# Performance work log

Measured on AMD Instinct MI355X. Metric: run time of the kernel, lower is better.

The kernel has to match this reference:

```python
import jax, jax.numpy as jnp
import numpy as np

N, E, F_IN, ED, H, C, G, ACT = 50000, 800000, 32, 5, 2, 32, 128, 8
HC = H * C


def _glorot(key, shape):
    fan_in, fan_out = shape[0], shape[-1]
    lim = (6.0 / (fan_in + fan_out)) ** 0.5
    return jax.random.uniform(key, shape, jnp.float32, -lim, lim)


def setup_inputs() -> dict:
    key = jax.random.key(0)
    ks = jax.random.split(key, 32)
    inp = {
        "x": jax.random.normal(ks[0], (N, F_IN), jnp.float32),
        "edge_index": jax.random.randint(ks[1], (2, E), 0, N, jnp.int64),
        "edge_attr": jax.random.normal(ks[2], (E, ED), jnp.float32),
        "batch": jnp.sort(jax.random.randint(ks[3], (N,), 0, G, jnp.int64)),
    }
    ki = 4
    for l, din in zip((1, 2, 3), (F_IN, HC, HC)):
        inp[f"W{l}"] = _glorot(ks[ki], (din, HC)); ki += 1
        inp[f"We{l}"] = _glorot(ks[ki], (ED, HC)); ki += 1
        inp[f"as{l}"] = _glorot(ks[ki], (H, C)); ki += 1
        inp[f"ad{l}"] = _glorot(ks[ki], (H, C)); ki += 1
        inp[f"ae{l}"] = _glorot(ks[ki], (H, C)); ki += 1
        inp[f"b{l}"] = jnp.zeros((HC,), jnp.float32)
    inp["Wl"] = _glorot(ks[ki], (HC, ACT)); ki += 1
    inp["bl"] = jnp.zeros((ACT,), jnp.float32)
    return inp


def _add_self_loops(edge_index, edge_attr):
    # PyG add_self_loops with fill_value='mean': self-loop edge_attr at node i
    # is the mean of edge_attr of edges whose dst is i (0 if none).
    dst = edge_index[1]
    deg = jax.ops.segment_sum(jnp.ones((E,), jnp.float32), dst, num_segments=N)
    loop_attr = jax.ops.segment_sum(edge_attr, dst, num_segments=N) / jnp.clip(deg, 1.0)[:, None]
    loops = jnp.arange(N, dtype=edge_index.dtype)
    ei = jnp.concatenate([edge_index, jnp.stack([loops, loops])], axis=1)
    ea = jnp.concatenate([edge_attr, loop_attr], axis=0)
    return ei, ea


def _gat_layer(x, src, dst, ea, W, We, a_s, a_d, a_e, b):
    xs = (x @ W).reshape(N, H, C)                      # node features per head
    e = (ea @ We).reshape(-1, H, C)                    # edge features per head
    a_src = jnp.einsum('nhc,hc->nh', xs, a_s)
    a_dst = jnp.einsum('nhc,hc->nh', xs, a_d)
    a_edge = jnp.einsum('ehc,hc->eh', e, a_e)
    logits = jax.nn.leaky_relu(a_src[src] + a_dst[dst] + a_edge, 0.2)  # [E',H]
    m = jax.ops.segment_max(logits, dst, num_segments=N)
    m = jnp.where(jnp.isfinite(m), m, 0.0)
    ex = jnp.exp(logits - m[dst])
    den = jax.ops.segment_sum(ex, dst, num_segments=N)
    alpha = ex / (den[dst] + 1e-16)
    msg = xs[src] * alpha[..., None]                   # [E',H,C]
    out = jax.ops.segment_sum(msg, dst, num_segments=N).reshape(N, HC)
    return out + b


def reference(x, edge_index, edge_attr, batch,
              W1, We1, as1, ad1, ae1, b1,
              W2, We2, as2, ad2, ae2, b2,
              W3, We3, as3, ad3, ae3, b3,
              Wl, bl):
    ei, ea = _add_self_loops(edge_index, edge_attr)
    src, dst = ei[0], ei[1]
    h = jax.nn.relu(_gat_layer(x, src, dst, ea, W1, We1, as1, ad1, ae1, b1))
    h = jax.nn.relu(_gat_layer(h, src, dst, ea, W2, We2, as2, ad2, ae2, b2))
    h = _gat_layer(h, src, dst, ea, W3, We3, as3, ad3, ae3, b3)
    # global mean pool over graphs
    cnt = jax.ops.segment_sum(jnp.ones((N,), jnp.float32), batch, num_segments=G)
    pooled = jax.ops.segment_sum(h, batch, num_segments=G) / jnp.clip(cnt, 1.0)[:, None]
    return jnp.tanh(pooled @ Wl + bl)
```

## Files before the change

kernel.cpp:

```cpp
#include <hip/hip_runtime.h>
#include <math.h>

#define N_NODES 50000
#define N_EDGES 800000
#define E_DIM   5
#define N_G     128
#define N_ACT   8
#define SBLK    512
#define SNB     ((N_NODES + SBLK - 1) / SBLK)


__global__ __launch_bounds__(256) void setup_kernel(
    const int* __restrict__ ei, const int* __restrict__ batch,
    const float* __restrict__ We1, const float* __restrict__ ae1,
    const float* __restrict__ We2, const float* __restrict__ ae2,
    const float* __restrict__ We3, const float* __restrict__ ae3,
    float* __restrict__ weff, int* __restrict__ gstart, int* __restrict__ hist) {
    int bid = blockIdx.x, tid = threadIdx.x;
    if (bid == 0) {
        if (tid <= N_G) {
            int g = tid, lo = 0, hi = N_NODES;
            while (lo < hi) { int mid = (lo + hi) >> 1; if (batch[mid] < g) lo = mid + 1; else hi = mid; }
            gstart[g] = lo;
        }
        int t = tid - 160;
        if (t >= 0 && t < 30) {
            int l = t / 10, r = t % 10, d = r >> 1, h = r & 1;
            const float* We = (l == 0) ? We1 : (l == 1) ? We2 : We3;
            const float* ae = (l == 0) ? ae1 : (l == 1) ? ae2 : ae3;
            float s = 0.f;
            for (int c = 0; c < 32; ++c) s += We[d * 64 + h * 32 + c] * ae[h * 32 + c];
            weff[l * 10 + d * 2 + h] = s;
        }
        return;
    }
    int k = (bid - 1) * 256 + tid;
    if (k < N_EDGES) atomicAdd(&hist[ei[N_EDGES + k]], 1);
}

__device__ __forceinline__ int wave_incl_scan(int v, int lane) {
    #pragma unroll
    for (int off = 1; off < 64; off <<= 1) {
        int n = __shfl_up(v, off);
        if (lane >= off) v += n;
    }
    return v;
}

__global__ __launch_bounds__(SBLK) void scan_bsum_kernel(const int* __restrict__ hist,
                                                         int* __restrict__ bsum) {
    int i = blockIdx.x * SBLK + threadIdx.x;
    int v = (i < N_NODES) ? hist[i] : 0;
    __shared__ int sm[SBLK / 64];
    int lane = threadIdx.x & 63, w = threadIdx.x >> 6;
    #pragma unroll
    for (int o = 32; o; o >>= 1) v += __shfl_xor(v, o);
    if (lane == 0) sm[w] = v;
    __syncthreads();
    if (threadIdx.x == 0) {
        int s = 0;
        #pragma unroll
        for (int k = 0; k < SBLK / 64; ++k) s += sm[k];
        bsum[blockIdx.x] = s;
    }
}

__global__ __launch_bounds__(SBLK) void scan_rowptr_kernel(const int* __restrict__ hist,
                                                           const int* __restrict__ bsum,
                                                           int* __restrict__ rowptr) {
    __shared__ int s_boffs;
    __shared__ int wtot[SBLK / 64];
    int bid = blockIdx.x;
    if (threadIdx.x < 64) {
        int v = 0;
        for (int i = threadIdx.x; i < bid; i += 64) v += bsum[i];
        #pragma unroll
        for (int o = 32; o; o >>= 1) v += __shfl_xor(v, o);
        if (threadIdx.x == 0) s_boffs = v;
    }
    int i = bid * SBLK + threadIdx.x;
    int v = (i < N_NODES) ? hist[i] : 0;
    int lane = threadIdx.x & 63, w = threadIdx.x >> 6;
    int inc = wave_incl_scan(v, lane);
    if (lane == 63) wtot[w] = inc;
    __syncthreads();
    int woff = 0;
    for (int k = 0; k < w; ++k) woff += wtot[k];
    int excl = s_boffs + woff + inc - v;
    if (i < N_NODES) rowptr[i] = excl;
    if (i == N_NODES - 1) rowptr[N_NODES] = excl + v;
}

__global__ void scatter_kernel(const int* __restrict__ ei, const float* __restrict__ ea,
                               const float* __restrict__ weff,
                               const int* __restrict__ rowptr, int* __restrict__ cur,
                               float* __restrict__ rec) {
    int k = blockIdx.x * blockDim.x + threadIdx.x;
    if (k >= N_EDGES) return;
    int s = ei[k], d = ei[N_EDGES + k];
    const float* ep = ea + (size_t)k * E_DIM;
    float e[5];
    #pragma unroll
    for (int j = 0; j < 5; ++j) e[j] = ep[j];
    float r[6] = {0.f, 0.f, 0.f, 0.f, 0.f, 0.f};
    #pragma unroll
    for (int j = 0; j < 5; ++j) {
        r[0] += e[j] * weff[j * 2];      r[1] += e[j] * weff[j * 2 + 1];
        r[2] += e[j] * weff[10 + j * 2]; r[3] += e[j] * weff[10 + j * 2 + 1];
        r[4] += e[j] * weff[20 + j * 2]; r[5] += e[j] * weff[20 + j * 2 + 1];
    }
    int pos = rowptr[d] + atomicAdd(&cur[d], 1);
    float4* rp = (float4*)(rec + (size_t)pos * 8);
    rp[0] = make_float4(r[0], r[1], r[2], r[3]);
    rp[1] = make_float4(r[4], r[5], __int_as_float(s), 0.f);
}


template <int DIN>
__global__ __launch_bounds__(256) void feat_kernel(
    const float* __restrict__ in, const float* __restrict__ W,
    const float* __restrict__ a_s, const float* __restrict__ a_d,
    float* __restrict__ xs, float* __restrict__ a_srcv, float* __restrict__ a_dstv) {
    __shared__ float Wl[DIN * 64];
    __shared__ float asl[64], adl[64];
    int tid = threadIdx.x;
    {
        const float4* Wg = (const float4*)W;
        float4* Wl4 = (float4*)Wl;
        #pragma unroll
        for (int i = tid; i < DIN * 16; i += 256) Wl4[i] = Wg[i];
        if (tid < 64) { asl[tid] = a_s[tid]; adl[tid] = a_d[tid]; }
    }
    __syncthreads();
    int n = blockIdx.x * 64 + (tid >> 2);
    int strip = tid & 3;
    if (n >= N_NODES) return;
    float4 xr[DIN / 4];
    const float4* row4 = (const float4*)(in + (size_t)n * DIN);
    #pragma unroll
    for (int k4 = 0; k4 < DIN / 4; ++k4) xr[k4] = row4[k4];
    float4 acc[4];
    #pragma unroll
    for (int j = 0; j < 4; ++j) acc[j] = make_float4(0.f, 0.f, 0.f, 0.f);
    const float4* W4 = (const float4*)Wl;
    #pragma unroll
    for (int k4 = 0; k4 < DIN / 4; ++k4) {
        float xk[4] = {xr[k4].x, xr[k4].y, xr[k4].z, xr[k4].w};
        #pragma unroll
        for (int kk = 0; kk < 4; ++kk) {
            int k = k4 * 4 + kk;
            #pragma unroll
            for (int j = 0; j < 4; ++j) {
                float4 w = W4[k * 16 + strip * 4 + j];
                acc[j].x += xk[kk] * w.x; acc[j].y += xk[kk] * w.y;
                acc[j].z += xk[kk] * w.z; acc[j].w += xk[kk] * w.w;
            }
        }
    }
    float ps = 0.f, pd = 0.f;
    #pragma unroll
    for (int j = 0; j < 4; ++j) {
        int c = strip * 16 + j * 4;
        ps += acc[j].x * asl[c] + acc[j].y * asl[c + 1] + acc[j].z * asl[c + 2] + acc[j].w * asl[c + 3];
        pd += acc[j].x * adl[c] + acc[j].y * adl[c + 1] + acc[j].z * adl[c + 2] + acc[j].w * adl[c + 3];
    }
    ps += __shfl_xor(ps, 1);
    pd += __shfl_xor(pd, 1);
    if ((strip & 1) == 0) {
        int h = strip >> 1;
        a_srcv[n * 2 + h] = ps;
        a_dstv[n * 2 + h] = pd;
    }
    float4* o = (float4*)(xs + (size_t)n * 64 + strip * 16);
    #pragma unroll
    for (int j = 0; j < 4; ++j) o[j] = acc[j];
}

template <int L>
__global__ __launch_bounds__(256) void node_agg_kernel(
    const int* __restrict__ rowptr, const float* __restrict__ rec,
    const float* __restrict__ a_srcv, const float* __restrict__ a_dstv,
    const float* __restrict__ xs, const float* __restrict__ b,
    float* __restrict__ out, int relu) {
    int nid = (blockIdx.x * 256 + threadIdx.x) >> 4;
    if (nid >= N_NODES) return;
    int lane = threadIdx.x & 63;
    int fl = lane & 15, h = fl >> 3;
    int gbase = lane & 48;
    int beg = rowptr[nid], end = rowptr[nid + 1];
    float2 ad2 = ((const float2*)a_dstv)[nid];

    float m0 = -INFINITY, m1 = -INFINITY, d0 = 0.f, d1 = 0.f;
    float aes0 = 0.f, aes1 = 0.f;
    for (int j = beg + fl; j < end; j += 16) {
        const float4* rp = (const float4*)(rec + (size_t)j * 8);
        float4 r0 = rp[0];
        float4 r1 = rp[1];
        int s = __float_as_int(r1.z);
        float aex = (L == 0) ? r0.x : (L == 1) ? r0.z : r1.x;
        float aey = (L == 0) ? r0.y : (L == 1) ? r0.w : r1.y;
        aes0 += aex; aes1 += aey;
        float2 as2 = ((const float2*)a_srcv)[s];
        float l0 = as2.x + ad2.x + aex;
        float l1 = as2.y + ad2.y + aey;
        l0 = (l0 > 0.f) ? l0 : 0.2f * l0;
        l1 = (l1 > 0.f) ? l1 : 0.2f * l1;
        float n0 = fmaxf(m0, l0);
        d0 = d0 * __expf(m0 - n0) + __expf(l0 - n0); m0 = n0;
        float n1 = fmaxf(m1, l1);
        d1 = d1 * __expf(m1 - n1) + __expf(l1 - n1); m1 = n1;
    }
    #pragma unroll
    for (int o = 8; o; o >>= 1) {
        float mo0 = __shfl_xor(m0, o), do0 = __shfl_xor(d0, o);
        float mo1 = __shfl_xor(m1, o), do1 = __shfl_xor(d1, o);
        float n0 = fmaxf(m0, mo0);
        float ea0 = (m0 == n0) ? 1.f : __expf(m0 - n0);
        float eb0 = (mo0 == n0) ? 1.f : __expf(mo0 - n0);
        d0 = d0 * ea0 + do0 * eb0; m0 = n0;
        float n1 = fmaxf(m1, mo1);
        float ea1 = (m1 == n1) ? 1.f : __expf(m1 - n1);
        float eb1 = (mo1 == n1) ? 1.f : __expf(mo1 - n1);
        d1 = d1 * ea1 + do1 * eb1; m1 = n1;
        aes0 += __shfl_xor(aes0, o);
        aes1 += __shfl_xor(aes1, o);
    }
    int ne = end - beg;
    float invne = 1.f / fmaxf((float)ne, 1.f);
    float2 as2n = ((const float2*)a_srcv)[nid];
    float ls0 = as2n.x + ad2.x + aes0 * invne;
    float ls1 = as2n.y + ad2.y + aes1 * invne;
    ls0 = (ls0 > 0.f) ? ls0 : 0.2f * ls0;
    ls1 = (ls1 > 0.f) ? ls1 : 0.2f * ls1;
    float M0 = fmaxf(m0, ls0), M1 = fmaxf(m1, ls1);
    float sc0 = (m0 == M0) ? 1.f : __expf(m0 - M0);
    float sc1 = (m1 == M1) ? 1.f : __expf(m1 - M1);
    float exS0 = __expf(ls0 - M0), exS1 = __expf(ls1 - M1);
    float den0 = d0 * sc0 + exS0;
    float den1 = d1 * sc1 + exS1;

    float4 acc = make_float4(0.f, 0.f, 0.f, 0.f);
    for (int cb = beg; cb < end; cb += 16) {
        int j = cb + fl;
        float ex0 = 0.f, ex1 = 0.f;
        int s = 0;
        if (j < end) {
            const float4* rp = (const float4*)(rec + (size_t)j * 8);
            float4 r0 = rp[0];
            float4 r1 = rp[1];
            s = __float_as_int(r1.z);
            float aex = (L == 0) ? r0.x : (L == 1) ? r0.z : r1.x;
            float aey = (L == 0) ? r0.y : (L == 1) ? r0.w : r1.y;
            float2 as2 = ((const float2*)a_srcv)[s];
            float l0 = as2.x + ad2.x + aex;
            float l1 = as2.y + ad2.y + aey;
            l0 = (l0 > 0.f) ? l0 : 0.2f * l0;
            l1 = (l1 > 0.f) ? l1 : 0.2f * l1;
            ex0 = __expf(l0 - M0);
            ex1 = __expf(l1 - M1);
        }
        int cnt = min(end - cb, 16);
        for (int t4 = 0; t4 < cnt; t4 += 4) {
            int tA = gbase + t4;
            float eA0 = __shfl(ex0, tA),     eA1 = __shfl(ex1, tA);     int sA = __shfl(s, tA);
            float eB0 = __shfl(ex0, tA + 1), eB1 = __shfl(ex1, tA + 1); int sB = __shfl(s, tA + 1);
            float eC0 = __shfl(ex0, tA + 2), eC1 = __shfl(ex1, tA + 2); int sC = __shfl(s, tA + 2);
            float eD0 = __shfl(ex0, tA + 3), eD1 = __shfl(ex1, tA + 3); int sD = __shfl(s, tA + 3);
            float eA = h ? eA1 : eA0, eB = h ? eB1 : eB0;
            float eC = h ? eC1 : eC0, eD = h ? eD1 : eD0;
            float4 xa = *(const float4*)(xs + (size_t)sA * 64 + fl * 4);
            float4 xb = *(const float4*)(xs + (size_t)sB * 64 + fl * 4);
            float4 xc = *(const float4*)(xs + (size_t)sC * 64 + fl * 4);
            float4 xd = *(const float4*)(xs + (size_t)sD * 64 + fl * 4);
            acc.x += eA * xa.x + eB * xb.x + eC * xc.x + eD * xd.x;
            acc.y += eA * xa.y + eB * xb.y + eC * xc.y + eD * xd.y;
            acc.z += eA * xa.z + eB * xb.z + eC * xc.z + eD * xd.z;
            acc.w += eA * xa.w + eB * xb.w + eC * xc.w + eD * xd.w;
        }
    }
    float exSh = h ? exS1 : exS0;
    float den  = (h ? den1 : den0) + 1e-16f;
    float4 xv = *(const float4*)(xs + (size_t)nid * 64 + fl * 4);
    float inv = 1.f / den;
    float4 b4 = ((const float4*)b)[fl];
    float4 v;
    v.x = (acc.x + exSh * xv.x) * inv + b4.x;
    v.y = (acc.y + exSh * xv.y) * inv + b4.y;
    v.z = (acc.z + exSh * xv.z) * inv + b4.z;
    v.w = (acc.w + exSh * xv.w) * inv + b4.w;
    if (relu) {
        v.x = fmaxf(v.x, 0.f); v.y = fmaxf(v.y, 0.f);
        v.z = fmaxf(v.z, 0.f); v.w = fmaxf(v.w, 0.f);
    }
    ((float4*)(out + (size_t)nid * 64))[fl] = v;
}


__global__ __launch_bounds__(256) void pool_head_kernel(
    const float* __restrict__ hfeat, const int* __restrict__ gstart,
    const float* __restrict__ Wl, const float* __restrict__ bl,
    float* __restrict__ out) {
    __shared__ float sm[4][64];
    __shared__ float pooledL[64];
    int g = blockIdx.x;
    int w = threadIdx.x >> 6, lane = threadIdx.x & 63;
    int beg = gstart[g], end = gstart[g + 1];
    float acc = 0.f;
    for (int n = beg + w; n < end; n += 4)
        acc += hfeat[(size_t)n * 64 + lane];
    sm[w][lane] = acc;
    __syncthreads();
    if (w == 0) {
        float v = sm[0][lane] + sm[1][lane] + sm[2][lane] + sm[3][lane];
        pooledL[lane] = v / fmaxf((float)(end - beg), 1.f);
    }
    __syncthreads();
    if (threadIdx.x < N_ACT) {
        int a = threadIdx.x;
        float s = bl[a];
        #pragma unroll
        for (int j = 0; j < 64; ++j) s += pooledL[j] * Wl[j * 8 + a];
        out[g * N_ACT + a] = tanhf(s);
    }
}

extern "C" void kernel_launch(void* const* d_in, const int* in_sizes, int n_in,
                              void* d_out, int out_size, void* d_ws, size_t ws_size,
                              hipStream_t stream) {
    const float* x    = (const float*)d_in[0];
    const int*   ei   = (const int*)d_in[1];
    const float* ea   = (const float*)d_in[2];
    const int*   batch= (const int*)d_in[3];
    const float* W[3]   = {(const float*)d_in[4],  (const float*)d_in[10], (const float*)d_in[16]};
    const float* We[3]  = {(const float*)d_in[5],  (const float*)d_in[11], (const float*)d_in[17]};
    const float* as_[3] = {(const float*)d_in[6],  (const float*)d_in[12], (const float*)d_in[18]};
    const float* ad_[3] = {(const float*)d_in[7],  (const float*)d_in[13], (const float*)d_in[19]};
    const float* ae_[3] = {(const float*)d_in[8],  (const float*)d_in[14], (const float*)d_in[20]};
    const float* b_[3]  = {(const float*)d_in[9],  (const float*)d_in[15], (const float*)d_in[21]};
    const float* Wlin = (const float*)d_in[22];
    const float* bl   = (const float*)d_in[23];
    float* out = (float*)d_out;

    float* ws = (float*)d_ws;
    size_t off = 0;
    float* A      = ws + off; off += (size_t)N_NODES * 64;
    float* B      = ws + off; off += (size_t)N_NODES * 64;
    float* rec    = ws + off; off += (size_t)N_EDGES * 8;
    float* a_srcv = ws + off; off += N_NODES * 2;
    float* a_dstv = ws + off; off += N_NODES * 2;
    float* weff   = ws + off; off += 32;
    int* rowptr = (int*)(ws + off); off += N_NODES + 1;
    int* hist   = (int*)(ws + off); off += N_NODES;
    int* cur    = (int*)(ws + off); off += N_NODES;
    int* gstart = (int*)(ws + off); off += N_G + 1;
    int* bsum   = (int*)(ws + off); off += SNB;

    hipMemsetAsync(hist, 0, 2 * N_NODES * sizeof(int), stream);
    setup_kernel<<<1 + (N_EDGES + 255) / 256, 256, 0, stream>>>(
        ei, batch, We[0], ae_[0], We[1], ae_[1], We[2], ae_[2], weff, gstart, hist);
    scan_bsum_kernel<<<SNB, SBLK, 0, stream>>>(hist, bsum);
    scan_rowptr_kernel<<<SNB, SBLK, 0, stream>>>(hist, bsum, rowptr);
    scatter_kernel<<<(N_EDGES + 255) / 256, 256, 0, stream>>>(ei, ea, weff, rowptr, cur, rec);

    const int NB = (N_NODES * 16 + 255) / 256;
    const int FB = (N_NODES + 63) / 64;
    for (int l = 0; l < 3; ++l) {
        if (l == 0)
            feat_kernel<32><<<FB, 256, 0, stream>>>(x, W[0], as_[0], ad_[0], B, a_srcv, a_dstv);
        else
            feat_kernel<64><<<FB, 256, 0, stream>>>(A, W[l], as_[l], ad_[l], B, a_srcv, a_dstv);
        if (l == 0)
            node_agg_kernel<0><<<NB, 256, 0, stream>>>(rowptr, rec, a_srcv, a_dstv, B, b_[0], A, 1);
        else if (l == 1)
            node_agg_kernel<1><<<NB, 256, 0, stream>>>(rowptr, rec, a_srcv, a_dstv, B, b_[1], A, 1);
        else
            node_agg_kernel<2><<<NB, 256, 0, stream>>>(rowptr, rec, a_srcv, a_dstv, B, b_[2], A, 0);
    }
    pool_head_kernel<<<N_G, 256, 0, stream>>>(A, gstart, Wlin, bl, out);
}
```

Before: 391.5 us.

## Store node features and edge records in fp16 to halve gather traffic

Projected node features xs are stored as fp16, and the per-edge CSR record shrinks from 32 bytes to 16 bytes by packing the three layers' edge attention terms as half2 pairs next to the source index. The aggregation kernels load these narrower values and unpack them to fp32 for accumulation. The scatter kernel now handles two edges per thread. This cuts memory traffic in the bandwidth-bound gather and softmax passes, at the cost of fp16 rounding error in features and edge logits.

```diff
diff --git a/kernel.cpp b/kernel.cpp
--- a/kernel.cpp
+++ b/kernel.cpp
@@ -1,8 +1,10 @@
 #include <hip/hip_runtime.h>
+#include <hip/hip_fp16.h>
 #include <math.h>
 
 #define N_NODES 50000
 #define N_EDGES 800000
+#define N_EH    400000
 #define E_DIM   5
 #define N_G     128
 #define N_ACT   8
@@ -94,25 +96,40 @@
 __global__ void scatter_kernel(const int* __restrict__ ei, const float* __restrict__ ea,
                                const float* __restrict__ weff,
                                const int* __restrict__ rowptr, int* __restrict__ cur,
-                               float* __restrict__ rec) {
-    int k = blockIdx.x * blockDim.x + threadIdx.x;
-    if (k >= N_EDGES) return;
-    int s = ei[k], d = ei[N_EDGES + k];
-    const float* ep = ea + (size_t)k * E_DIM;
-    float e[5];
-    #pragma unroll
-    for (int j = 0; j < 5; ++j) e[j] = ep[j];
-    float r[6] = {0.f, 0.f, 0.f, 0.f, 0.f, 0.f};
+                               int4* __restrict__ rec) {
+    int k1 = blockIdx.x * blockDim.x + threadIdx.x;
+    if (k1 >= N_EH) return;
+    int k2 = k1 + N_EH;
+    int s1 = ei[k1], d1 = ei[N_EDGES + k1];
+    int s2 = ei[k2], d2 = ei[N_EDGES + k2];
+    const float* e1 = ea + (size_t)k1 * E_DIM;
+    const float* e2 = ea + (size_t)k2 * E_DIM;
+    float r1[6] = {0, 0, 0, 0, 0, 0}, r2[6] = {0, 0, 0, 0, 0, 0};
     #pragma unroll
     for (int j = 0; j < 5; ++j) {
-        r[0] += e[j] * weff[j * 2];      r[1] += e[j] * weff[j * 2 + 1];
-        r[2] += e[j] * weff[10 + j * 2]; r[3] += e[j] * weff[10 + j * 2 + 1];
-        r[4] += e[j] * weff[20 + j * 2]; r[5] += e[j] * weff[20 + j * 2 + 1];
-    }
-    int pos = rowptr[d] + atomicAdd(&cur[d], 1);
-    float4* rp = (float4*)(rec + (size_t)pos * 8);
-    rp[0] = make_float4(r[0], r[1], r[2], r[3]);
-    rp[1] = make_float4(r[4], r[5], __int_as_float(s), 0.f);
+        float a = e1[j], b = e2[j];
+        #pragma unroll
+        for (int q = 0; q < 3; ++q) {
+            r1[2 * q]     += a * weff[10 * q + j * 2];
+            r1[2 * q + 1] += a * weff[10 * q + j * 2 + 1];
+            r2[2 * q]     += b * weff[10 * q + j * 2];
+            r2[2 * q + 1] += b * weff[10 * q + j * 2 + 1];
+        }
+    }
+    union { __half2 h; int i; } u;
+    int4 v1, v2;
+    u.h = __floats2half2_rn(r1[0], r1[1]); v1.x = u.i;
+    u.h = __floats2half2_rn(r1[2], r1[3]); v1.y = u.i;
+    u.h = __floats2half2_rn(r1[4], r1[5]); v1.z = u.i;
+    v1.w = s1;
+    u.h = __floats2half2_rn(r2[0], r2[1]); v2.x = u.i;
+    u.h = __floats2half2_rn(r2[2], r2[3]); v2.y = u.i;
+    u.h = __floats2half2_rn(r2[4], r2[5]); v2.z = u.i;
+    v2.w = s2;
+    int p1 = rowptr[d1] + atomicAdd(&cur[d1], 1);
+    int p2 = rowptr[d2] + atomicAdd(&cur[d2], 1);
+    rec[p1] = v1;
+    rec[p2] = v2;
 }
 
 
@@ -120,7 +137,7 @@
 __global__ __launch_bounds__(256) void feat_kernel(
     const float* __restrict__ in, const float* __restrict__ W,
     const float* __restrict__ a_s, const float* __restrict__ a_d,
-    float* __restrict__ xs, float* __restrict__ a_srcv, float* __restrict__ a_dstv) {
+    __half* __restrict__ xs, float* __restrict__ a_srcv, float* __restrict__ a_dstv) {
     __shared__ float Wl[DIN * 64];
     __shared__ float asl[64], adl[64];
     int tid = threadIdx.x;
@@ -171,16 +188,27 @@
         a_srcv[n * 2 + h] = ps;
         a_dstv[n * 2 + h] = pd;
     }
-    float4* o = (float4*)(xs + (size_t)n * 64 + strip * 16);
-    #pragma unroll
-    for (int j = 0; j < 4; ++j) o[j] = acc[j];
+    union { __half2 h[8]; int4 v[2]; } pk;
+    #pragma unroll
+    for (int j = 0; j < 4; ++j) {
+        pk.h[2 * j]     = __floats2half2_rn(acc[j].x, acc[j].y);
+        pk.h[2 * j + 1] = __floats2half2_rn(acc[j].z, acc[j].w);
+    }
+    int4* o = (int4*)(xs + (size_t)n * 64 + strip * 16);
+    o[0] = pk.v[0];
+    o[1] = pk.v[1];
+}
+
+__device__ __forceinline__ float2 h2f(int bits) {
+    union { int i; __half2 h; } u; u.i = bits;
+    return __half22float2(u.h);
 }
 
 template <int L>
 __global__ __launch_bounds__(256) void node_agg_kernel(
-    const int* __restrict__ rowptr, const float* __restrict__ rec,
+    const int* __restrict__ rowptr, const int4* __restrict__ rec,
     const float* __restrict__ a_srcv, const float* __restrict__ a_dstv,
-    const float* __restrict__ xs, const float* __restrict__ b,
+    const __half* __restrict__ xs, const float* __restrict__ b,
     float* __restrict__ out, int relu) {
     int nid = (blockIdx.x * 256 + threadIdx.x) >> 4;
     if (nid >= N_NODES) return;
@@ -193,16 +221,13 @@
     float m0 = -INFINITY, m1 = -INFINITY, d0 = 0.f, d1 = 0.f;
     float aes0 = 0.f, aes1 = 0.f;
     for (int j = beg + fl; j < end; j += 16) {
-        const float4* rp = (const float4*)(rec + (size_t)j * 8);
-        float4 r0 = rp[0];
-        float4 r1 = rp[1];
-        int s = __float_as_int(r1.z);
-        float aex = (L == 0) ? r0.x : (L == 1) ? r0.z : r1.x;
-        float aey = (L == 0) ? r0.y : (L == 1) ? r0.w : r1.y;
-        aes0 += aex; aes1 += aey;
+        int4 rv = rec[j];
+        float2 aep = h2f((L == 0) ? rv.x : (L == 1) ? rv.y : rv.z);
+        int s = rv.w;
+        aes0 += aep.x; aes1 += aep.y;
         float2 as2 = ((const float2*)a_srcv)[s];
-        float l0 = as2.x + ad2.x + aex;
-        float l1 = as2.y + ad2.y + aey;
+        float l0 = as2.x + ad2.x + aep.x;
+        float l1 = as2.y + ad2.y + aep.y;
         l0 = (l0 > 0.f) ? l0 : 0.2f * l0;
         l1 = (l1 > 0.f) ? l1 : 0.2f * l1;
         float n0 = fmaxf(m0, l0);
@@ -245,15 +270,12 @@
         float ex0 = 0.f, ex1 = 0.f;
         int s = 0;
         if (j < end) {
-            const float4* rp = (const float4*)(rec + (size_t)j * 8);
-            float4 r0 = rp[0];
-            float4 r1 = rp[1];
-            s = __float_as_int(r1.z);
-            float aex = (L == 0) ? r0.x : (L == 1) ? r0.z : r1.x;
-            float aey = (L == 0) ? r0.y : (L == 1) ? r0.w : r1.y;
+            int4 rv = rec[j];
+            float2 aep = h2f((L == 0) ? rv.x : (L == 1) ? rv.y : rv.z);
+            s = rv.w;
             float2 as2 = ((const float2*)a_srcv)[s];
-            float l0 = as2.x + ad2.x + aex;
-            float l1 = as2.y + ad2.y + aey;
+            float l0 = as2.x + ad2.x + aep.x;
+            float l1 = as2.y + ad2.y + aep.y;
             l0 = (l0 > 0.f) ? l0 : 0.2f * l0;
             l1 = (l1 > 0.f) ? l1 : 0.2f * l1;
             ex0 = __expf(l0 - M0);
@@ -268,26 +290,31 @@
             float eD0 = __shfl(ex0, tA + 3), eD1 = __shfl(ex1, tA + 3); int sD = __shfl(s, tA + 3);
             float eA = h ? eA1 : eA0, eB = h ? eB1 : eB0;
             float eC = h ? eC1 : eC0, eD = h ? eD1 : eD0;
-            float4 xa = *(const float4*)(xs + (size_t)sA * 64 + fl * 4);
-            float4 xb = *(const float4*)(xs + (size_t)sB * 64 + fl * 4);
-            float4 xc = *(const float4*)(xs + (size_t)sC * 64 + fl * 4);
-            float4 xd = *(const float4*)(xs + (size_t)sD * 64 + fl * 4);
-            acc.x += eA * xa.x + eB * xb.x + eC * xc.x + eD * xd.x;
-            acc.y += eA * xa.y + eB * xb.y + eC * xc.y + eD * xd.y;
-            acc.z += eA * xa.z + eB * xb.z + eC * xc.z + eD * xd.z;
-            acc.w += eA * xa.w + eB * xb.w + eC * xc.w + eD * xd.w;
+            int2 xa = *(const int2*)(xs + (size_t)sA * 64 + fl * 4);
+            int2 xb = *(const int2*)(xs + (size_t)sB * 64 + fl * 4);
+            int2 xc = *(const int2*)(xs + (size_t)sC * 64 + fl * 4);
+            int2 xd = *(const int2*)(xs + (size_t)sD * 64 + fl * 4);
+            float2 a0 = h2f(xa.x), a1 = h2f(xa.y);
+            float2 b0 = h2f(xb.x), b1 = h2f(xb.y);
+            float2 c0 = h2f(xc.x), c1 = h2f(xc.y);
+            float2 d0v = h2f(xd.x), d1v = h2f(xd.y);
+            acc.x += eA * a0.x + eB * b0.x + eC * c0.x + eD * d0v.x;
+            acc.y += eA * a0.y + eB * b0.y + eC * c0.y + eD * d0v.y;
+            acc.z += eA * a1.x + eB * b1.x + eC * c1.x + eD * d1v.x;
+            acc.w += eA * a1.y + eB * b1.y + eC * c1.y + eD * d1v.y;
         }
     }
     float exSh = h ? exS1 : exS0;
     float den  = (h ? den1 : den0) + 1e-16f;
-    float4 xv = *(const float4*)(xs + (size_t)nid * 64 + fl * 4);
+    int2 xv = *(const int2*)(xs + (size_t)nid * 64 + fl * 4);
+    float2 s0 = h2f(xv.x), s1 = h2f(xv.y);
     float inv = 1.f / den;
     float4 b4 = ((const float4*)b)[fl];
     float4 v;
-    v.x = (acc.x + exSh * xv.x) * inv + b4.x;
-    v.y = (acc.y + exSh * xv.y) * inv + b4.y;
-    v.z = (acc.z + exSh * xv.z) * inv + b4.z;
-    v.w = (acc.w + exSh * xv.w) * inv + b4.w;
+    v.x = (acc.x + exSh * s0.x) * inv + b4.x;
+    v.y = (acc.y + exSh * s0.y) * inv + b4.y;
+    v.z = (acc.z + exSh * s1.x) * inv + b4.z;
+    v.w = (acc.w + exSh * s1.y) * inv + b4.w;
     if (relu) {
         v.x = fmaxf(v.x, 0.f); v.y = fmaxf(v.y, 0.f);
         v.z = fmaxf(v.z, 0.f); v.w = fmaxf(v.w, 0.f);
@@ -344,8 +371,8 @@
     float* ws = (float*)d_ws;
     size_t off = 0;
     float* A      = ws + off; off += (size_t)N_NODES * 64;
-    float* B      = ws + off; off += (size_t)N_NODES * 64;
-    float* rec    = ws + off; off += (size_t)N_EDGES * 8;
+    __half* xs16  = (__half*)(ws + off); off += (size_t)N_NODES * 32;
+    int4* rec     = (int4*)(ws + off); off += (size_t)N_EDGES * 4;
     float* a_srcv = ws + off; off += N_NODES * 2;
     float* a_dstv = ws + off; off += N_NODES * 2;
     float* weff   = ws + off; off += 32;
@@ -360,21 +387,21 @@
         ei, batch, We[0], ae_[0], We[1], ae_[1], We[2], ae_[2], weff, gstart, hist);
     scan_bsum_kernel<<<SNB, SBLK, 0, stream>>>(hist, bsum);
     scan_rowptr_kernel<<<SNB, SBLK, 0, stream>>>(hist, bsum, rowptr);
-    scatter_kernel<<<(N_EDGES + 255) / 256, 256, 0, stream>>>(ei, ea, weff, rowptr, cur, rec);
+    scatter_kernel<<<(N_EH + 255) / 256, 256, 0, stream>>>(ei, ea, weff, rowptr, cur, rec);
 
     const int NB = (N_NODES * 16 + 255) / 256;
     const int FB = (N_NODES + 63) / 64;
     for (int l = 0; l < 3; ++l) {
         if (l == 0)
-            feat_kernel<32><<<FB, 256, 0, stream>>>(x, W[0], as_[0], ad_[0], B, a_srcv, a_dstv);
+            feat_kernel<32><<<FB, 256, 0, stream>>>(x, W[0], as_[0], ad_[0], xs16, a_srcv, a_dstv);
         else
-            feat_kernel<64><<<FB, 256, 0, stream>>>(A, W[l], as_[l], ad_[l], B, a_srcv, a_dstv);
+            feat_kernel<64><<<FB, 256, 0, stream>>>(A, W[l], as_[l], ad_[l], xs16, a_srcv, a_dstv);
         if (l == 0)
-            node_agg_kernel<0><<<NB, 256, 0, stream>>>(rowptr, rec, a_srcv, a_dstv, B, b_[0], A, 1);
+            node_agg_kernel<0><<<NB, 256, 0, stream>>>(rowptr, rec, a_srcv, a_dstv, xs16, b_[0], A, 1);
         else if (l == 1)
-            node_agg_kernel<1><<<NB, 256, 0, stream>>>(rowptr, rec, a_srcv, a_dstv, B, b_[1], A, 1);
+            node_agg_kernel<1><<<NB, 256, 0, stream>>>(rowptr, rec, a_srcv, a_dstv, xs16, b_[1], A, 1);
         else
-            node_agg_kernel<2><<<NB, 256, 0, stream>>>(rowptr, rec, a_srcv, a_dstv, B, b_[2], A, 0);
+            node_agg_kernel<2><<<NB, 256, 0, stream>>>(rowptr, rec, a_srcv, a_dstv, xs16, b_[2], A, 0);
     }
     pool_head_kernel<<<N_G, 256, 0, stream>>>(A, gstart, Wlin, bl, out);
 }
```

Result: faster. 344.8 us (-11.9%).
